# Optimization experiments

Measured on AMD Instinct MI355X. Metric: run time of the kernel, lower is better.

## Reference

```python
import jax, jax.numpy as jnp
import numpy as np

D_IN = 1024
D_OUT = 1024
NUM_HEADS = 16
HEAD_DIM = D_OUT // NUM_HEADS


def setup_inputs() -> dict:
    key = jax.random.key(0)
    k_x, k_qkv, k_pw, k_pb = jax.random.split(key, 4)
    x = jax.random.normal(k_x, (2, 2048, D_IN), dtype=jnp.float32)
    # torch nn.Linear(d_in, 3*d_out, bias=False): weight [3*d_out, d_in]
    w_qkv = jax.random.normal(k_qkv, (3 * D_OUT, D_IN), dtype=jnp.float32) * (1.0 / np.sqrt(D_IN))
    # proj: nn.Linear(d_out, d_out) with bias
    w_proj = jax.random.normal(k_pw, (D_OUT, D_OUT), dtype=jnp.float32) * (1.0 / np.sqrt(D_OUT))
    b_proj = jax.random.normal(k_pb, (D_OUT,), dtype=jnp.float32) * 0.01
    return {"x": x, "w_qkv": w_qkv, "w_proj": w_proj, "b_proj": b_proj}


def reference(x, w_qkv, w_proj, b_proj):
    B, S, _ = x.shape
    # fused QKV projection: [B,S,3*D_OUT]
    qkv = jnp.einsum('bsd,ed->bse', x, w_qkv)
    qkv = qkv.reshape(B, S, 3, NUM_HEADS, HEAD_DIM)
    q, k, v = jnp.moveaxis(qkv, 2, 0)  # each [B,S,H,Dh]
    scale = 1.0 / jnp.sqrt(jnp.asarray(HEAD_DIM, dtype=x.dtype))
    # scores [B,H,S,S]
    scores = jnp.einsum('bqhd,bkhd->bhqk', q, k) * scale
    causal = jnp.tril(jnp.ones((S, S), dtype=bool))
    scores = jnp.where(causal, scores, jnp.asarray(-jnp.inf, dtype=scores.dtype))
    attn = jax.nn.softmax(scores, axis=-1)
    ctx = jnp.einsum('bhqk,bkhd->bqhd', attn, v)  # [B,S,H,Dh]
    ctx = ctx.reshape(B, S, D_OUT)
    return jnp.einsum('bsd,ed->bse', ctx, w_proj) + b_proj
```

## Files before the change

### kernel.cpp

```cpp
#include <hip/hip_runtime.h>
#include <hip/hip_bf16.h>
#include <cstdint>

#define B_SZ   2
#define S_LEN  2048
#define NH     16
#define LDA    72

using f32x4 = __attribute__((ext_vector_type(4))) float;
typedef __bf16 bf16x8 __attribute__((ext_vector_type(8)));
typedef __bf16 bf16x4 __attribute__((ext_vector_type(4)));

__device__ inline float bf2f(unsigned short u) {
    union { unsigned int i; float f; } v; v.i = ((unsigned int)u) << 16; return v.f;
}
__device__ inline unsigned short f2bf(float f) {
    union { float f; unsigned int i; } v; v.f = f;
    unsigned int r = v.i + 0x7fff + ((v.i >> 16) & 1);
    return (unsigned short)(r >> 16);
}
__device__ inline f32x4 mfma16(bf16x8 a, bf16x8 b, f32x4 c) {
    return __builtin_amdgcn_mfma_f32_16x16x32_bf16(a, b, c, 0, 0, 0);
}
__device__ inline unsigned pack_bf16x2(float lo, float hi) {
    float2 f2; f2.x = lo; f2.y = hi;
    __hip_bfloat162 bb = __float22bfloat162_rn(f2);
    union { __hip_bfloat162 b; unsigned u; } cv; cv.b = bb;
    return cv.u;
}
__device__ inline void ldsbar() {
    __builtin_amdgcn_sched_barrier(0);
    asm volatile("s_waitcnt lgkmcnt(0)" ::: "memory");
    __builtin_amdgcn_s_barrier();
    __builtin_amdgcn_sched_barrier(0);
}
__device__ inline void stC(float* C, size_t idx, float v)  { C[idx] = v; }
__device__ inline void stC(__bf16* C, size_t idx, float v) { ((unsigned short*)C)[idx] = f2bf(v); }

#define QSF (0.125f * 1.4426950408889634f)

__global__ __launch_bounds__(256) void f2b3_kernel(
    const float* __restrict__ a, int na4, __bf16* __restrict__ outa,
    const float* __restrict__ b, int nb4, __bf16* __restrict__ outb,
    const float* __restrict__ c, int nc4, __bf16* __restrict__ outc)
{
    int i = blockIdx.x * blockDim.x + threadIdx.x;
    const float* src; __bf16* dst; int idx;
    if (i < na4)                  { src = a; dst = outa; idx = i; }
    else if (i < na4 + nb4)       { src = b; dst = outb; idx = i - na4; }
    else if (i < na4 + nb4 + nc4) { src = c; dst = outc; idx = i - na4 - nb4; }
    else return;
    float4 v = ((const float4*)src)[idx];
    ushort4 o;
    o.x = f2bf(v.x); o.y = f2bf(v.y); o.z = f2bf(v.z); o.w = f2bf(v.w);
    ((ushort4*)dst)[idx] = o;
}

template <typename TO, int HAS_BIAS, int QSCALE>
__global__ __launch_bounds__(256) void gemm128(
    const __bf16* __restrict__ A, const __bf16* __restrict__ W,
    const float* __restrict__ bias, TO* __restrict__ C,
    int M, int N, int K)
{
    __shared__ __bf16 Alds[3][128 * 32];
    __shared__ __bf16 Blds[3][128 * 32];
    const int tid  = threadIdx.x, lane = tid & 63, w = tid >> 6;
    const int c16  = lane & 15, quad = lane >> 4;
    const int mBase = blockIdx.y * 128, nBase = blockIdx.x * 128;
    const int moff = (w & 1) * 64, noff = (w >> 1) * 64;

    f32x4 acc[4][4];
#pragma unroll
    for (int i = 0; i < 4; ++i)
#pragma unroll
        for (int j = 0; j < 4; ++j) acc[i][j] = (f32x4){0.f, 0.f, 0.f, 0.f};

    auto stage = [&](int buf, int k0) {
#pragma unroll
        for (int p = 0; p < 2; ++p) {
            const int linear = p * 256 + tid;
            const int row = linear >> 2;
            const int seg = (linear & 3) ^ (row & 3);
            const int lbase = (p * 256 + w * 64) * 8;
            const __bf16* ga = A + (size_t)(mBase + row) * K + k0 + seg * 8;
            const __bf16* gb = W + (size_t)(nBase + row) * K + k0 + seg * 8;
            __builtin_amdgcn_global_load_lds(
                (const __attribute__((address_space(1))) void*)ga,
                (__attribute__((address_space(3))) void*)(&Alds[buf][lbase]), 16, 0, 0);
            __builtin_amdgcn_global_load_lds(
                (const __attribute__((address_space(1))) void*)gb,
                (__attribute__((address_space(3))) void*)(&Blds[buf][lbase]), 16, 0, 0);
        }
    };

    stage(0, 0);
    if (32 < K) stage(1, 32);
    int cur = 0;
    for (int k0 = 0; k0 < K; k0 += 32) {
        __builtin_amdgcn_sched_barrier(0);
        if (k0 + 32 < K) asm volatile("s_waitcnt vmcnt(4) lgkmcnt(0)" ::: "memory");
        else             asm volatile("s_waitcnt vmcnt(0) lgkmcnt(0)" ::: "memory");
        __builtin_amdgcn_s_barrier();
        __builtin_amdgcn_sched_barrier(0);

        if (k0 + 64 < K) stage(cur == 0 ? 2 : cur - 1, k0 + 64);

        bf16x8 af[4], bw[4];
#pragma unroll
        for (int i = 0; i < 4; ++i) {
            const int rowA = moff + i * 16 + c16;
            af[i] = *(const bf16x8*)&Alds[cur][rowA * 32 + ((quad ^ (rowA & 3)) << 3)];
            const int rowB = noff + i * 16 + c16;
            bw[i] = *(const bf16x8*)&Blds[cur][rowB * 32 + ((quad ^ (rowB & 3)) << 3)];
        }
#pragma unroll
        for (int i = 0; i < 4; ++i)
#pragma unroll
            for (int j = 0; j < 4; ++j)
                acc[i][j] = mfma16(af[i], bw[j], acc[i][j]);
        cur = (cur == 2) ? 0 : cur + 1;
    }

#pragma unroll
    for (int j = 0; j < 4; ++j) {
        const int colBase = nBase + noff + j * 16;
        const float qs = (QSCALE && colBase < 1024) ? QSF : 1.0f;
        const int col = colBase + c16;
        const float bv = HAS_BIAS ? bias[col] : 0.f;
#pragma unroll
        for (int i = 0; i < 4; ++i)
#pragma unroll
            for (int r = 0; r < 4; ++r) {
                const int row = mBase + moff + i * 16 + quad * 4 + r;
                stC(C, (size_t)row * N + col, acc[i][j][r] * qs + bv);
            }
    }
}

template <typename TO, int HAS_BIAS>
__global__ __launch_bounds__(256) void gemm64(
    const __bf16* __restrict__ A, const __bf16* __restrict__ W,
    const float* __restrict__ bias, TO* __restrict__ C,
    int M, int N, int K)
{
    __shared__ __bf16 Alds[3][64 * 32];
    __shared__ __bf16 Blds[3][128 * 32];
    const int tid  = threadIdx.x, lane = tid & 63, w = tid >> 6;
    const int c16  = lane & 15, quad = lane >> 4;
    const int mBase = blockIdx.y * 64, nBase = blockIdx.x * 128;
    const int moff = (w & 1) * 32, noff = (w >> 1) * 64;

    f32x4 acc[2][4];
#pragma unroll
    for (int i = 0; i < 2; ++i)
#pragma unroll
        for (int j = 0; j < 4; ++j) acc[i][j] = (f32x4){0.f, 0.f, 0.f, 0.f};

    auto stage = [&](int buf, int k0) {
        {
            const int row = tid >> 2;
            const int seg = (tid & 3) ^ (row & 3);
            const int lbase = (w * 64) * 8;
            const __bf16* ga = A + (size_t)(mBase + row) * K + k0 + seg * 8;
            __builtin_amdgcn_global_load_lds(
                (const __attribute__((address_space(1))) void*)ga,
                (__attribute__((address_space(3))) void*)(&Alds[buf][lbase]), 16, 0, 0);
        }
#pragma unroll
        for (int p = 0; p < 2; ++p) {
            const int linear = p * 256 + tid;
            const int row = linear >> 2;
            const int seg = (linear & 3) ^ (row & 3);
            const int lbase = (p * 256 + w * 64) * 8;
            const __bf16* gb = W + (size_t)(nBase + row) * K + k0 + seg * 8;
            __builtin_amdgcn_global_load_lds(
                (const __attribute__((address_space(1))) void*)gb,
                (__attribute__((address_space(3))) void*)(&Blds[buf][lbase]), 16, 0, 0);
        }
    };

    stage(0, 0);
    if (32 < K) stage(1, 32);
    int cur = 0;
    for (int k0 = 0; k0 < K; k0 += 32) {
        __builtin_amdgcn_sched_barrier(0);
        if (k0 + 32 < K) asm volatile("s_waitcnt vmcnt(3) lgkmcnt(0)" ::: "memory");
        else             asm volatile("s_waitcnt vmcnt(0) lgkmcnt(0)" ::: "memory");
        __builtin_amdgcn_s_barrier();
        __builtin_amdgcn_sched_barrier(0);

        if (k0 + 64 < K) stage(cur == 0 ? 2 : cur - 1, k0 + 64);

        bf16x8 af[2], bw[4];
#pragma unroll
        for (int i = 0; i < 2; ++i) {
            const int rowA = moff + i * 16 + c16;
            af[i] = *(const bf16x8*)&Alds[cur][rowA * 32 + ((quad ^ (rowA & 3)) << 3)];
        }
#pragma unroll
        for (int j = 0; j < 4; ++j) {
            const int rowB = noff + j * 16 + c16;
            bw[j] = *(const bf16x8*)&Blds[cur][rowB * 32 + ((quad ^ (rowB & 3)) << 3)];
        }
#pragma unroll
        for (int i = 0; i < 2; ++i)
#pragma unroll
            for (int j = 0; j < 4; ++j)
                acc[i][j] = mfma16(af[i], bw[j], acc[i][j]);
        cur = (cur == 2) ? 0 : cur + 1;
    }

#pragma unroll
    for (int j = 0; j < 4; ++j) {
        const int col = nBase + noff + j * 16 + c16;
        const float bv = HAS_BIAS ? bias[col] : 0.f;
#pragma unroll
        for (int i = 0; i < 2; ++i)
#pragma unroll
            for (int r = 0; r < 4; ++r) {
                const int row = mBase + moff + i * 16 + quad * 4 + r;
                stC(C, (size_t)row * N + col, acc[i][j][r] + bv);
            }
    }
}

__global__ __launch_bounds__(256) void attn(
    const __bf16* __restrict__ qkv, __bf16* __restrict__ ctx)
{
    __shared__ __bf16 Qs[64 * LDA];
    __shared__ __bf16 Ks[64 * LDA];
    __shared__ __bf16 Vs[64 * LDA];

    const int tid  = threadIdx.x;
    const int lane = tid & 63;
    const int w    = tid >> 6;
    const int c16  = lane & 15;
    const int quad = lane >> 4;
    const int bh = blockIdx.x, b = bh >> 4, h = bh & 15;
    const int y  = blockIdx.y;

    const int a  = y & 7, uq = y >> 3;
    const int qt = (uq == 0) ? (31 - a) : (uq == 1) ? (16 + a)
                 : (uq == 2) ? (15 - a) : a;
    const int c1 = qt + 1;
    const int qBase = qt * 64;

    const int krow0 = tid >> 3;
    const int kd0   = (tid & 7) * 8;
    const int u     = tid & 31;
    const int dblk  = tid >> 5;
    const int vcol  = 32 * (u & 1) + 8 * ((u >> 1) & 3) + 2 * (u >> 3);

    const size_t rowB = (size_t)b * S_LEN;

    const __bf16* kp0 = qkv + (rowB + krow0) * 3072 + 1024 + h * 64 + kd0;
    const __bf16* kp1 = kp0 + (size_t)32 * 3072;
    const __bf16* vp0 = qkv + (rowB + 2 * u) * 3072 + 2048 + h * 64 + dblk * 8;
    const __bf16* vp1 = vp0 + (size_t)3072;

    uint4 kr0 = *(const uint4*)kp0;
    uint4 kr1 = *(const uint4*)kp1;
    uint4 vr0 = *(const uint4*)vp0;
    uint4 vr1 = *(const uint4*)vp1;

#pragma unroll
    for (int p = 0; p < 2; ++p) {
        const int linear = p * 256 + tid;
        const int row = linear >> 3;
        const int d0 = (linear & 7) * 8;
        const __bf16* g = qkv + (rowB + qBase + row) * 3072 + h * 64 + d0;
        *(uint4*)&Qs[row * LDA + d0] = *(const uint4*)g;
    }
    ldsbar();

    const bf16x8 aq0 = *(const bf16x8*)&Qs[(w * 16 + c16) * LDA + quad * 8];
    const bf16x8 aq1 = *(const bf16x8*)&Qs[(w * 16 + c16) * LDA + 32 + quad * 8];

    float lp = 0.f;
    f32x4 acc_o[4];
#pragma unroll
    for (int j = 0; j < 4; ++j) acc_o[j] = (f32x4){0.f, 0.f, 0.f, 0.f};

    for (int cc = 0; cc < c1; ++cc) {
        *(uint4*)&Ks[krow0 * LDA + kd0]        = kr0;
        *(uint4*)&Ks[(krow0 + 32) * LDA + kd0] = kr1;
        {
            const unsigned short* e1 = (const unsigned short*)&vr0;
            const unsigned short* e2 = (const unsigned short*)&vr1;
#pragma unroll
            for (int d = 0; d < 8; ++d) {
                const unsigned pack = (unsigned)e1[d] | ((unsigned)e2[d] << 16);
                *(unsigned*)&Vs[(dblk * 8 + d) * LDA + vcol] = pack;
            }
        }
        ldsbar();

        if (cc + 1 < c1) {
            kp0 += (size_t)64 * 3072; kp1 += (size_t)64 * 3072;
            vp0 += (size_t)64 * 3072; vp1 += (size_t)64 * 3072;
            kr0 = *(const uint4*)kp0;
            kr1 = *(const uint4*)kp1;
            vr0 = *(const uint4*)vp0;
            vr1 = *(const uint4*)vp1;
        }

        f32x4 sc[4];
#pragma unroll
        for (int j = 0; j < 4; ++j) sc[j] = (f32x4){0.f, 0.f, 0.f, 0.f};
        __builtin_amdgcn_s_setprio(1);
#pragma unroll
        for (int j = 0; j < 4; ++j) {
            bf16x8 bk0 = *(const bf16x8*)&Ks[(j * 16 + c16) * LDA + quad * 8];
            bf16x8 bk1 = *(const bf16x8*)&Ks[(j * 16 + c16) * LDA + 32 + quad * 8];
            sc[j] = mfma16(bk0, aq0, sc[j]);
            sc[j] = mfma16(bk1, aq1, sc[j]);
        }
        __builtin_amdgcn_s_setprio(0);

        if (cc == qt) {
            const int q = qBase + w * 16 + c16;
#pragma unroll
            for (int j = 0; j < 4; ++j) {
#pragma unroll
                for (int r = 0; r < 4; ++r) {
                    const int key = cc * 64 + j * 16 + quad * 4 + r;
                    if (key > q) sc[j][r] = -1e30f;
                }
            }
        }

        float p_[4][4];
#pragma unroll
        for (int j = 0; j < 4; ++j)
#pragma unroll
            for (int r = 0; r < 4; ++r)
                p_[j][r] = exp2f(sc[j][r]);
#pragma unroll
        for (int j = 0; j < 4; ++j)
            lp += (p_[j][0] + p_[j][1]) + (p_[j][2] + p_[j][3]);

        union { unsigned uu[4]; bf16x8 v; } B0, B1;
#pragma unroll
        for (int j = 0; j < 4; ++j) {
            B0.uu[j] = pack_bf16x2(p_[j][0], p_[j][1]);
            B1.uu[j] = pack_bf16x2(p_[j][2], p_[j][3]);
        }
        const bf16x8 bp0 = B0.v;
        const bf16x8 bp1 = B1.v;

        __builtin_amdgcn_s_setprio(1);
#pragma unroll
        for (int jd = 0; jd < 4; ++jd) {
            bf16x8 av0 = *(const bf16x8*)&Vs[(jd * 16 + c16) * LDA + quad * 8];
            bf16x8 av1 = *(const bf16x8*)&Vs[(jd * 16 + c16) * LDA + 32 + quad * 8];
            acc_o[jd] = mfma16(av0, bp0, acc_o[jd]);
            acc_o[jd] = mfma16(av1, bp1, acc_o[jd]);
        }
        __builtin_amdgcn_s_setprio(0);
        ldsbar();
    }

    lp += __shfl_xor(lp, 16);
    lp += __shfl_xor(lp, 32);

    const float inv = 1.0f / lp;
    const size_t rowO = (rowB + qBase + w * 16 + c16) * 1024 + h * 64;
#pragma unroll
    for (int jd = 0; jd < 4; ++jd) {
        bf16x4 ov;
#pragma unroll
        for (int r = 0; r < 4; ++r) ov[r] = (__bf16)(acc_o[jd][r] * inv);
        *(bf16x4*)&ctx[rowO + jd * 16 + quad * 4] = ov;
    }
}

extern "C" void kernel_launch(void* const* d_in, const int* in_sizes, int n_in,
                              void* d_out, int out_size, void* d_ws, size_t ws_size,
                              hipStream_t stream) {
    const float* x      = (const float*)d_in[0];
    const float* w_qkv  = (const float*)d_in[1];
    const float* w_proj = (const float*)d_in[2];
    const float* b_proj = (const float*)d_in[3];
    float* out = (float*)d_out;

    __bf16* qkvb = (__bf16*)d_ws;
    __bf16* xb   = qkvb + (size_t)4096 * 3072;
    __bf16* wqb  = xb + (size_t)4096 * 1024;
    __bf16* wpb  = wqb + (size_t)3072 * 1024;
    __bf16* ctxb = xb;

    const int M = B_SZ * S_LEN;
    const int nx4 = 4096 * 1024 / 4, nq4 = 3072 * 1024 / 4, np4 = 1024 * 1024 / 4;

    f2b3_kernel<<<(nx4 + nq4 + np4 + 255) / 256, 256, 0, stream>>>(
        x, nx4, xb, w_qkv, nq4, wqb, w_proj, np4, wpb);

    gemm128<__bf16, 0, 1><<<dim3(3072 / 128, M / 128), 256, 0, stream>>>(
        xb, wqb, nullptr, qkvb, M, 3072, 1024);

    attn<<<dim3(B_SZ * NH, 32), 256, 0, stream>>>(qkvb, ctxb);

    gemm64<float, 1><<<dim3(1024 / 128, M / 64), 256, 0, stream>>>(
        ctxb, wpb, b_proj, out, M, 1024, 1024);
}
```

Before: 175.0 us.

## Process two adjacent query tiles per attention block to share K/V loads

Each attention block now has 512 threads covering two adjacent 64-row query tiles (2p+1 and 2p), so every K/V tile staged in shared memory is reused by eight waves instead of four. Grid y drops to 16, and pairs are ordered to balance causal work. Waves of the lower tile skip the final K/V tile but still take part in the barriers, so some threads sit idle on that last step. Per-thread global load width for K/V is halved.

```diff
diff --git a/kernel.cpp b/kernel.cpp
--- a/kernel.cpp
+++ b/kernel.cpp
@@ -224,10 +224,10 @@
     }
 }
 
-__global__ __launch_bounds__(256) void attn(
+__global__ __launch_bounds__(512) void attn(
     const __bf16* __restrict__ qkv, __bf16* __restrict__ ctx)
 {
-    __shared__ __bf16 Qs[64 * LDA];
+    __shared__ __bf16 Qs[128 * LDA];
     __shared__ __bf16 Ks[64 * LDA];
     __shared__ __bf16 Vs[64 * LDA];
 
@@ -237,44 +237,45 @@
     const int c16  = lane & 15;
     const int quad = lane >> 4;
     const int bh = blockIdx.x, b = bh >> 4, h = bh & 15;
-    const int y  = blockIdx.y;
-
-    const int a  = y & 7, uq = y >> 3;
-    const int qt = (uq == 0) ? (31 - a) : (uq == 1) ? (16 + a)
-                 : (uq == 2) ? (15 - a) : a;
-    const int c1 = qt + 1;
-    const int qBase = qt * 64;
-
-    const int krow0 = tid >> 3;
-    const int kd0   = (tid & 7) * 8;
-    const int u     = tid & 31;
-    const int dblk  = tid >> 5;
-    const int vcol  = 32 * (u & 1) + 8 * ((u >> 1) & 3) + 2 * (u >> 3);
+    const int py = blockIdx.y;
+
+    const int p    = (py < 8) ? py : 23 - py;
+    const int qtA  = 2 * p + 1, qtB = 2 * p;
+    const int tileSel = w >> 2, wl = w & 3;
+    const int qt_w  = tileSel ? qtB : qtA;
+    const int qBase = qt_w * 64;
+    const int c1 = qtA + 1;
+
+    const int krow = tid >> 3;
+    const int kd0  = (tid & 7) * 8;
+    const int u    = tid & 31;
+    const int dsel = tid >> 5;
+    const int vcol = 32 * (u & 1) + 8 * ((u >> 1) & 3) + 2 * (u >> 3);
 
     const size_t rowB = (size_t)b * S_LEN;
 
-    const __bf16* kp0 = qkv + (rowB + krow0) * 3072 + 1024 + h * 64 + kd0;
-    const __bf16* kp1 = kp0 + (size_t)32 * 3072;
-    const __bf16* vp0 = qkv + (rowB + 2 * u) * 3072 + 2048 + h * 64 + dblk * 8;
+    const __bf16* kp  = qkv + (rowB + krow) * 3072 + 1024 + h * 64 + kd0;
+    const __bf16* vp0 = qkv + (rowB + 2 * u) * 3072 + 2048 + h * 64 + dsel * 4;
     const __bf16* vp1 = vp0 + (size_t)3072;
 
-    uint4 kr0 = *(const uint4*)kp0;
-    uint4 kr1 = *(const uint4*)kp1;
-    uint4 vr0 = *(const uint4*)vp0;
-    uint4 vr1 = *(const uint4*)vp1;
-
-#pragma unroll
-    for (int p = 0; p < 2; ++p) {
-        const int linear = p * 256 + tid;
+    uint4 kr  = *(const uint4*)kp;
+    uint2 vr0 = *(const uint2*)vp0;
+    uint2 vr1 = *(const uint2*)vp1;
+
+#pragma unroll
+    for (int p2 = 0; p2 < 2; ++p2) {
+        const int linear = p2 * 512 + tid;
         const int row = linear >> 3;
-        const int d0 = (linear & 7) * 8;
-        const __bf16* g = qkv + (rowB + qBase + row) * 3072 + h * 64 + d0;
+        const int d0  = (linear & 7) * 8;
+        const int grow = (row < 64) ? (qtA * 64 + row) : (qtB * 64 + (row - 64));
+        const __bf16* g = qkv + (rowB + grow) * 3072 + h * 64 + d0;
         *(uint4*)&Qs[row * LDA + d0] = *(const uint4*)g;
     }
     ldsbar();
 
-    const bf16x8 aq0 = *(const bf16x8*)&Qs[(w * 16 + c16) * LDA + quad * 8];
-    const bf16x8 aq1 = *(const bf16x8*)&Qs[(w * 16 + c16) * LDA + 32 + quad * 8];
+    const int qrow = tileSel * 64 + wl * 16 + c16;
+    const bf16x8 aq0 = *(const bf16x8*)&Qs[qrow * LDA + quad * 8];
+    const bf16x8 aq1 = *(const bf16x8*)&Qs[qrow * LDA + 32 + quad * 8];
 
     float lp = 0.f;
     f32x4 acc_o[4];
@@ -282,81 +283,81 @@
     for (int j = 0; j < 4; ++j) acc_o[j] = (f32x4){0.f, 0.f, 0.f, 0.f};
 
     for (int cc = 0; cc < c1; ++cc) {
-        *(uint4*)&Ks[krow0 * LDA + kd0]        = kr0;
-        *(uint4*)&Ks[(krow0 + 32) * LDA + kd0] = kr1;
+        *(uint4*)&Ks[krow * LDA + kd0] = kr;
         {
             const unsigned short* e1 = (const unsigned short*)&vr0;
             const unsigned short* e2 = (const unsigned short*)&vr1;
 #pragma unroll
-            for (int d = 0; d < 8; ++d) {
-                const unsigned pack = (unsigned)e1[d] | ((unsigned)e2[d] << 16);
-                *(unsigned*)&Vs[(dblk * 8 + d) * LDA + vcol] = pack;
+            for (int d = 0; d < 4; ++d) {
+                const unsigned pk = (unsigned)e1[d] | ((unsigned)e2[d] << 16);
+                *(unsigned*)&Vs[(dsel * 4 + d) * LDA + vcol] = pk;
             }
         }
         ldsbar();
 
         if (cc + 1 < c1) {
-            kp0 += (size_t)64 * 3072; kp1 += (size_t)64 * 3072;
+            kp  += (size_t)64 * 3072;
             vp0 += (size_t)64 * 3072; vp1 += (size_t)64 * 3072;
-            kr0 = *(const uint4*)kp0;
-            kr1 = *(const uint4*)kp1;
-            vr0 = *(const uint4*)vp0;
-            vr1 = *(const uint4*)vp1;
-        }
-
-        f32x4 sc[4];
-#pragma unroll
-        for (int j = 0; j < 4; ++j) sc[j] = (f32x4){0.f, 0.f, 0.f, 0.f};
-        __builtin_amdgcn_s_setprio(1);
-#pragma unroll
-        for (int j = 0; j < 4; ++j) {
-            bf16x8 bk0 = *(const bf16x8*)&Ks[(j * 16 + c16) * LDA + quad * 8];
-            bf16x8 bk1 = *(const bf16x8*)&Ks[(j * 16 + c16) * LDA + 32 + quad * 8];
-            sc[j] = mfma16(bk0, aq0, sc[j]);
-            sc[j] = mfma16(bk1, aq1, sc[j]);
-        }
-        __builtin_amdgcn_s_setprio(0);
-
-        if (cc == qt) {
-            const int q = qBase + w * 16 + c16;
+            kr  = *(const uint4*)kp;
+            vr0 = *(const uint2*)vp0;
+            vr1 = *(const uint2*)vp1;
+        }
+
+        if (cc <= qt_w) {
+            f32x4 sc[4];
+#pragma unroll
+            for (int j = 0; j < 4; ++j) sc[j] = (f32x4){0.f, 0.f, 0.f, 0.f};
+            __builtin_amdgcn_s_setprio(1);
 #pragma unroll
             for (int j = 0; j < 4; ++j) {
-#pragma unroll
-                for (int r = 0; r < 4; ++r) {
-                    const int key = cc * 64 + j * 16 + quad * 4 + r;
-                    if (key > q) sc[j][r] = -1e30f;
+                bf16x8 bk0 = *(const bf16x8*)&Ks[(j * 16 + c16) * LDA + quad * 8];
+                bf16x8 bk1 = *(const bf16x8*)&Ks[(j * 16 + c16) * LDA + 32 + quad * 8];
+                sc[j] = mfma16(bk0, aq0, sc[j]);
+                sc[j] = mfma16(bk1, aq1, sc[j]);
+            }
+            __builtin_amdgcn_s_setprio(0);
+
+            if (cc == qt_w) {
+                const int q = qBase + wl * 16 + c16;
+#pragma unroll
+                for (int j = 0; j < 4; ++j) {
+#pragma unroll
+                    for (int r = 0; r < 4; ++r) {
+                        const int key = cc * 64 + j * 16 + quad * 4 + r;
+                        if (key > q) sc[j][r] = -1e30f;
+                    }
                 }
             }
-        }
-
-        float p_[4][4];
-#pragma unroll
-        for (int j = 0; j < 4; ++j)
-#pragma unroll
-            for (int r = 0; r < 4; ++r)
-                p_[j][r] = exp2f(sc[j][r]);
-#pragma unroll
-        for (int j = 0; j < 4; ++j)
-            lp += (p_[j][0] + p_[j][1]) + (p_[j][2] + p_[j][3]);
-
-        union { unsigned uu[4]; bf16x8 v; } B0, B1;
-#pragma unroll
-        for (int j = 0; j < 4; ++j) {
-            B0.uu[j] = pack_bf16x2(p_[j][0], p_[j][1]);
-            B1.uu[j] = pack_bf16x2(p_[j][2], p_[j][3]);
-        }
-        const bf16x8 bp0 = B0.v;
-        const bf16x8 bp1 = B1.v;
-
-        __builtin_amdgcn_s_setprio(1);
-#pragma unroll
-        for (int jd = 0; jd < 4; ++jd) {
-            bf16x8 av0 = *(const bf16x8*)&Vs[(jd * 16 + c16) * LDA + quad * 8];
-            bf16x8 av1 = *(const bf16x8*)&Vs[(jd * 16 + c16) * LDA + 32 + quad * 8];
-            acc_o[jd] = mfma16(av0, bp0, acc_o[jd]);
-            acc_o[jd] = mfma16(av1, bp1, acc_o[jd]);
-        }
-        __builtin_amdgcn_s_setprio(0);
+
+            float p_[4][4];
+#pragma unroll
+            for (int j = 0; j < 4; ++j)
+#pragma unroll
+                for (int r = 0; r < 4; ++r)
+                    p_[j][r] = exp2f(sc[j][r]);
+#pragma unroll
+            for (int j = 0; j < 4; ++j)
+                lp += (p_[j][0] + p_[j][1]) + (p_[j][2] + p_[j][3]);
+
+            union { unsigned uu[4]; bf16x8 v; } B0, B1;
+#pragma unroll
+            for (int j = 0; j < 4; ++j) {
+                B0.uu[j] = pack_bf16x2(p_[j][0], p_[j][1]);
+                B1.uu[j] = pack_bf16x2(p_[j][2], p_[j][3]);
+            }
+            const bf16x8 bp0 = B0.v;
+            const bf16x8 bp1 = B1.v;
+
+            __builtin_amdgcn_s_setprio(1);
+#pragma unroll
+            for (int jd = 0; jd < 4; ++jd) {
+                bf16x8 av0 = *(const bf16x8*)&Vs[(jd * 16 + c16) * LDA + quad * 8];
+                bf16x8 av1 = *(const bf16x8*)&Vs[(jd * 16 + c16) * LDA + 32 + quad * 8];
+                acc_o[jd] = mfma16(av0, bp0, acc_o[jd]);
+                acc_o[jd] = mfma16(av1, bp1, acc_o[jd]);
+            }
+            __builtin_amdgcn_s_setprio(0);
+        }
         ldsbar();
     }
 
@@ -364,7 +365,7 @@
     lp += __shfl_xor(lp, 32);
 
     const float inv = 1.0f / lp;
-    const size_t rowO = (rowB + qBase + w * 16 + c16) * 1024 + h * 64;
+    const size_t rowO = (rowB + qBase + wl * 16 + c16) * 1024 + h * 64;
 #pragma unroll
     for (int jd = 0; jd < 4; ++jd) {
         bf16x4 ov;
@@ -398,7 +399,7 @@
     gemm128<__bf16, 0, 1><<<dim3(3072 / 128, M / 128), 256, 0, stream>>>(
         xb, wqb, nullptr, qkvb, M, 3072, 1024);
 
-    attn<<<dim3(B_SZ * NH, 32), 256, 0, stream>>>(qkvb, ctxb);
+    attn<<<dim3(B_SZ * NH, 16), 512, 0, stream>>>(qkvb, ctxb);
 
     gemm64<float, 1><<<dim3(1024 / 128, M / 64), 256, 0, stream>>>(
         ctxb, wpb, b_proj, out, M, 1024, 1024);
```

New measurement: 197.2 us. 12.7% more time.
